# Kernel tuning notes

Measured on AMD Instinct MI355X. Metric: run time of the kernel, lower is better.

## Reference

```python
import jax, jax.numpy as jnp
import numpy as np
from jax.ops import segment_sum, segment_max

N = 40000   # total nodes
E = 160000  # directed edges (before self-loops)
B = 1024    # graphs in batch
FXD = 78    # node feature dim
H = 10      # GAT heads
DOUT = 128  # fc_g1 output dim
DP = 256    # protein feature dim


def setup_inputs() -> dict:
    key = jax.random.key(0)
    ks = jax.random.split(key, 32)
    w = lambda i, shape: jax.random.normal(ks[i], shape, dtype=jnp.float32) * 0.05
    inp = {}
    inp['x'] = jax.random.normal(ks[0], (N, FXD), dtype=jnp.float32)
    inp['edge_index'] = jax.random.randint(ks[1], (2, E), 0, N)
    inp['batch'] = jnp.sort(jax.random.randint(ks[2], (N,), 0, B))
    inp['protein_vec'] = jax.random.normal(ks[3], (B, 1, DP), dtype=jnp.float32)
    # protein_fc
    inp['pfc_w'] = w(4, (DP, DP)); inp['pfc_b'] = w(5, (DP,))
    # GATConv(78 -> 78, heads=10, concat)
    inp['gat_w'] = w(6, (FXD, H * FXD))
    inp['gat_att_src'] = w(7, (H, FXD)); inp['gat_att_dst'] = w(8, (H, FXD))
    inp['gat_b'] = w(9, (H * FXD,))
    # GCNConv(780 -> 780)
    inp['gcn_w'] = w(10, (H * FXD, H * FXD)); inp['gcn_b'] = w(11, (H * FXD,))
    # fc_g1 780 -> 128
    inp['fcg1_w'] = w(12, (H * FXD, DOUT)); inp['fcg1_b'] = w(13, (DOUT,))
    # cross attention projections (d_head = 128)
    inp['q_w'] = w(14, (DOUT, 128)); inp['q_b'] = w(15, (128,))
    inp['k_w'] = w(16, (DP, 128)); inp['k_b'] = w(17, (128,))
    inp['v_w'] = w(18, (DP, DOUT)); inp['v_b'] = w(19, (DOUT,))
    # head MLP
    inp['fc1_w'] = w(20, (DOUT + DP, 1024)); inp['fc1_b'] = w(21, (1024,))
    inp['fc2_w'] = w(22, (1024, 512)); inp['fc2_b'] = w(23, (512,))
    inp['out_w'] = w(24, (512, 1)); inp['out_b'] = w(25, (1,))
    return inp


def _add_self_loops(edge_index):
    loops = jnp.arange(N)
    src = jnp.concatenate([edge_index[0], loops])
    dst = jnp.concatenate([edge_index[1], loops])
    return src, dst


def _gat_conv(x, src, dst, W, a_src, a_dst, b):
    # PyG GATConv: per-head linear, edge attention softmax over dst neighborhoods
    h = (x @ W).reshape(N, H, FXD)                     # [N,H,C]
    asrc = (h * a_src).sum(-1)                          # [N,H]
    adst = (h * a_dst).sum(-1)                          # [N,H]
    alpha = jax.nn.leaky_relu(asrc[src] + adst[dst], 0.2)  # [Etot,H]
    m = segment_max(alpha, dst, num_segments=N)
    e = jnp.exp(alpha - m[dst])
    s = segment_sum(e, dst, num_segments=N)
    attn = e / (s[dst] + 1e-16)
    out = segment_sum(attn[:, :, None] * h[src], dst, num_segments=N)
    return out.reshape(N, H * FXD) + b


def _gcn_conv(x, src, dst, W, b):
    # PyG GCNConv with self-loops and symmetric normalization
    deg = segment_sum(jnp.ones_like(dst, dtype=x.dtype), dst, num_segments=N)
    dinv = jnp.where(deg > 0, deg ** -0.5, 0.0)
    norm = dinv[src] * dinv[dst]                        # [Etot]
    h = x @ W
    return segment_sum(norm[:, None] * h[src], dst, num_segments=N) + b


def reference(x, edge_index, batch, protein_vec, pfc_w, pfc_b, gat_w, gat_att_src,
              gat_att_dst, gat_b, gcn_w, gcn_b, fcg1_w, fcg1_b, q_w, q_b, k_w, k_b,
              v_w, v_b, fc1_w, fc1_b, fc2_w, fc2_b, out_w, out_b):
    relu = jax.nn.relu
    src, dst = _add_self_loops(edge_index)
    pv = relu(protein_vec.squeeze(1) @ pfc_w + pfc_b)   # [B,256] (dropout = eval identity)
    h = relu(_gat_conv(x, src, dst, gat_w, gat_att_src, gat_att_dst, gat_b))
    drug_nodes = relu(_gcn_conv(h, src, dst, gcn_w, gcn_b))          # [N,780]
    dn = relu(drug_nodes @ fcg1_w + fcg1_b)                           # [N,128]
    # cross attention: per-node score against its graph's protein vector
    q = dn @ q_w + q_b                                  # [N,128]
    k = pv @ k_w + k_b                                  # [B,128]
    v = pv @ v_w + v_b                                  # [B,128]
    scores = (q * k[batch]).sum(1, keepdims=True) / jnp.sqrt(128.0)   # [N,1]
    m = segment_max(scores, batch, num_segments=B)
    e = jnp.exp(scores - m[batch])
    s = segment_sum(e, batch, num_segments=B)
    attn = e / s[batch]
    attended = dn + attn * v[batch]                     # [N,128]
    pooled = segment_max(attended, batch, num_segments=B)             # [B,128]
    pooled = jnp.where(jnp.isfinite(pooled), pooled, 0.0)
    xc = jnp.concatenate([pooled, pv], axis=1)          # [B,384]
    h1 = relu(xc @ fc1_w + fc1_b)
    h2 = relu(h1 @ fc2_w + fc2_b)
    return h2 @ out_w + out_b                           # [B,1]
```

## Files before the change

kernel.cpp:

```cpp
#include <hip/hip_runtime.h>
#include <hip/hip_bf16.h>
#include <math.h>

#define N_NODES 40000
#define E_EDGES 160000
#define ETOT    (E_EDGES + N_NODES)
#define B_GRAPH 1024
#define FXD     78
#define H_HEADS 10
#define HF      (H_HEADS * FXD)
#define HF_LD   800
#define XK_LD   96
#define DOUT    128
#define DP      256
#define SCAN_TILES 40

typedef __hip_bfloat16 bf16;
typedef __attribute__((ext_vector_type(8))) short short8;
typedef __attribute__((ext_vector_type(4))) float f32x4;

static __device__ __forceinline__ void storev(float* p, float v) { *p = v; }
static __device__ __forceinline__ void storev(bf16* p, float v) { *p = __float2bfloat16(v); }

static __device__ __forceinline__ ushort f2b_bits(float v) {
    bf16 b = __float2bfloat16(v);
    return *reinterpret_cast<ushort*>(&b);
}
static __device__ __forceinline__ float b2f_bits(short u) {
    return __uint_as_float(((unsigned)(unsigned short)u) << 16);
}

__global__ void k_f2b_pad(const float* __restrict__ in, bf16* __restrict__ out,
                          int M, int K, int ldk) {
    int i = blockIdx.x * blockDim.x + threadIdx.x;
    if (i >= M * ldk) return;
    int r = i / ldk, k = i - r * ldk;
    out[i] = __float2bfloat16((k < K) ? in[(size_t)r * K + k] : 0.f);
}

__global__ void k_f2bt_t(const float* __restrict__ w, bf16* __restrict__ wt,
                         int K, int N, int ldk) {
    __shared__ float tile[32][33];
    const int kt = blockIdx.x * 32;
    const int nt = blockIdx.y * 32;
    const int tx = threadIdx.x & 31, ty = threadIdx.x >> 5;
#pragma unroll
    for (int i = 0; i < 32; i += 8) {
        int k = kt + ty + i, n = nt + tx;
        tile[ty + i][tx] = (k < K && n < N) ? w[(size_t)k * N + n] : 0.f;
    }
    __syncthreads();
#pragma unroll
    for (int i = 0; i < 32; i += 8) {
        int n = nt + ty + i, k = kt + tx;
        if (n < N && k < ldk) wt[(size_t)n * ldk + k] = __float2bfloat16(tile[tx][ty + i]);
    }
}

__global__ void k_eff(const float* __restrict__ gat_w, const float* __restrict__ aw_s,
                      const float* __restrict__ aw_d, bf16* __restrict__ wt_E) {
    int idx = blockIdx.x * blockDim.x + threadIdx.x;
    if (idx >= 20 * XK_LD) return;
    int row = idx / XK_LD, f = idx - row * XK_LD;
    float acc = 0.f;
    if (f < FXD) {
        int h = row % H_HEADS;
        const float* aw = (row < H_HEADS) ? aw_s : aw_d;
        const float* wp = gat_w + (size_t)f * HF + h * FXD;
        const float* ap = aw + h * FXD;
        for (int c = 0; c < FXD; c++) acc += wp[c] * ap[c];
    }
    wt_E[idx] = __float2bfloat16(acc);
}

template <typename OutT, int BIAS, int RELU>
__global__ __launch_bounds__(256)
void mfma_mm(const ushort* __restrict__ A, int lda, const ushort* __restrict__ WT, int ldb,
             const float* __restrict__ bias, OutT* __restrict__ C, int ldc,
             int M, int K, int N) {
    const int RT = (M + 127) >> 7;
    const int CT = (N + 127) >> 7;
    const int p = blockIdx.x;
    const int r = (p & 7) + 8 * (p / (8 * CT));
    const int c = (p >> 3) % CT;
    if (r >= RT) return;
    const int m0 = r * 128;
    const int n0 = c * 128;

    __shared__ ushort As[128 * 40];
    __shared__ ushort Bs[128 * 40];
    const int tid = threadIdx.x;
    const int wave = tid >> 6, lane = tid & 63;
    const int quad = lane >> 4, l16 = lane & 15;
    const int wr = (wave & 1) * 64;
    const int wc = (wave >> 1) * 64;

    f32x4 acc[4][4];
#pragma unroll
    for (int mi = 0; mi < 4; mi++)
#pragma unroll
        for (int ni = 0; ni < 4; ni++) acc[mi][ni] = (f32x4){0.f, 0.f, 0.f, 0.f};

    const int ar = tid >> 1;
    const int ak = (tid & 1) * 16;

    int grow = m0 + ar; if (grow >= M) grow = M - 1;
    int gn   = n0 + ar; if (gn >= N)   gn = N - 1;
    const ushort* arow = A  + (size_t)grow * lda + ak;
    const ushort* brow = WT + (size_t)gn * ldb + ak;

    uint4 a0 = *(const uint4*)(arow);
    uint4 a1 = *(const uint4*)(arow + 8);
    uint4 b0 = *(const uint4*)(brow);
    uint4 b1 = *(const uint4*)(brow + 8);

    for (int kb = 0; kb < K; kb += 32) {
        *(uint4*)&As[ar * 40 + ak]     = a0;
        *(uint4*)&As[ar * 40 + ak + 8] = a1;
        *(uint4*)&Bs[ar * 40 + ak]     = b0;
        *(uint4*)&Bs[ar * 40 + ak + 8] = b1;
        __syncthreads();
        if (kb + 32 < K) {
            a0 = *(const uint4*)(arow + kb + 32);
            a1 = *(const uint4*)(arow + kb + 40);
            b0 = *(const uint4*)(brow + kb + 32);
            b1 = *(const uint4*)(brow + kb + 40);
        }
        short8 af[4], bfr[4];
#pragma unroll
        for (int mi = 0; mi < 4; mi++)
            af[mi] = *(const short8*)&As[(wr + mi * 16 + l16) * 40 + quad * 8];
#pragma unroll
        for (int ni = 0; ni < 4; ni++)
            bfr[ni] = *(const short8*)&Bs[(wc + ni * 16 + l16) * 40 + quad * 8];
#pragma unroll
        for (int mi = 0; mi < 4; mi++)
#pragma unroll
            for (int ni = 0; ni < 4; ni++)
                acc[mi][ni] = __builtin_amdgcn_mfma_f32_16x16x32_bf16(
                    af[mi], bfr[ni], acc[mi][ni], 0, 0, 0);
        __syncthreads();
    }
#pragma unroll
    for (int mi = 0; mi < 4; mi++)
#pragma unroll
        for (int ni = 0; ni < 4; ni++)
#pragma unroll
            for (int rg = 0; rg < 4; rg++) {
                int row = m0 + wr + mi * 16 + quad * 4 + rg;
                int col = n0 + wc + ni * 16 + l16;
                if (row < M && col < N) {
                    float v = acc[mi][ni][rg];
                    if (BIAS) v += bias[col];
                    if (RELU) v = fmaxf(v, 0.f);
                    storev(&C[(size_t)row * ldc + col], v);
                }
            }
}

static inline int mm_grid(int M, int N) {
    int RT = (M + 127) >> 7, CT = (N + 127) >> 7;
    int RTpad = ((RT + 7) >> 3) << 3;
    return RTpad * CT;
}

template <typename OutT, int BIAS, int RELU>
__global__ __launch_bounds__(256)
void mfma_mm64(const ushort* __restrict__ A, int lda, const ushort* __restrict__ WT, int ldb,
               const float* __restrict__ bias, OutT* __restrict__ C, int ldc,
               int M, int K, int N) {
    const int RT = (M + 63) >> 6;
    const int CT = (N + 127) >> 7;
    const int p = blockIdx.x;
    const int r = (p & 7) + 8 * (p / (8 * CT));
    const int c = (p >> 3) % CT;
    if (r >= RT) return;
    const int m0 = r * 64;
    const int n0 = c * 128;

    __shared__ ushort As[64 * 40];
    __shared__ ushort Bs[128 * 40];
    const int tid = threadIdx.x;
    const int wave = tid >> 6, lane = tid & 63;
    const int quad = lane >> 4, l16 = lane & 15;
    const int wc = wave * 32;

    f32x4 acc[4][2];
#pragma unroll
    for (int mi = 0; mi < 4; mi++)
#pragma unroll
        for (int ni = 0; ni < 2; ni++) acc[mi][ni] = (f32x4){0.f, 0.f, 0.f, 0.f};

    const int ar  = tid >> 2, aak = (tid & 3) * 8;
    const int br  = tid >> 1, bak = (tid & 1) * 16;

    int grow = m0 + ar; if (grow >= M) grow = M - 1;
    int gn   = n0 + br; if (gn >= N)   gn = N - 1;
    const ushort* arow = A  + (size_t)grow * lda + aak;
    const ushort* brow = WT + (size_t)gn * ldb + bak;

    uint4 a0 = *(const uint4*)(arow);
    uint4 b0 = *(const uint4*)(brow);
    uint4 b1 = *(const uint4*)(brow + 8);

    for (int kb = 0; kb < K; kb += 32) {
        *(uint4*)&As[ar * 40 + aak]     = a0;
        *(uint4*)&Bs[br * 40 + bak]     = b0;
        *(uint4*)&Bs[br * 40 + bak + 8] = b1;
        __syncthreads();
        if (kb + 32 < K) {
            a0 = *(const uint4*)(arow + kb + 32);
            b0 = *(const uint4*)(brow + kb + 32);
            b1 = *(const uint4*)(brow + kb + 40);
        }
        short8 af[4], bfr[2];
#pragma unroll
        for (int mi = 0; mi < 4; mi++)
            af[mi] = *(const short8*)&As[(mi * 16 + l16) * 40 + quad * 8];
#pragma unroll
        for (int ni = 0; ni < 2; ni++)
            bfr[ni] = *(const short8*)&Bs[(wc + ni * 16 + l16) * 40 + quad * 8];
#pragma unroll
        for (int mi = 0; mi < 4; mi++)
#pragma unroll
            for (int ni = 0; ni < 2; ni++)
                acc[mi][ni] = __builtin_amdgcn_mfma_f32_16x16x32_bf16(
                    af[mi], bfr[ni], acc[mi][ni], 0, 0, 0);
        __syncthreads();
    }
#pragma unroll
    for (int mi = 0; mi < 4; mi++)
#pragma unroll
        for (int ni = 0; ni < 2; ni++)
#pragma unroll
            for (int rg = 0; rg < 4; rg++) {
                int row = m0 + mi * 16 + quad * 4 + rg;
                int col = n0 + wc + ni * 16 + l16;
                if (row < M && col < N) {
                    float v = acc[mi][ni][rg];
                    if (BIAS) v += bias[col];
                    if (RELU) v = fmaxf(v, 0.f);
                    storev(&C[(size_t)row * ldc + col], v);
                }
            }
}

static inline int mm_grid64(int M, int N) {
    int RT = (M + 63) >> 6, CT = (N + 127) >> 7;
    int RTpad = ((RT + 7) >> 3) << 3;
    return RTpad * CT;
}

__global__ void k_pv(const float* __restrict__ pvec, const float* __restrict__ w,
                     const float* __restrict__ b, float* __restrict__ pv) {
    __shared__ float sm[DP];
    int bg = blockIdx.x, t = threadIdx.x;
    sm[t] = pvec[(size_t)bg * DP + t];
    __syncthreads();
    float acc = 0.f;
    for (int k = 0; k < DP; k++) acc += sm[k] * w[(size_t)k * DP + t];
    pv[(size_t)bg * DP + t] = fmaxf(acc + b[t], 0.f);
}

__global__ void k_kv(const float* __restrict__ pv,
                     const float* __restrict__ kw, const float* __restrict__ kb,
                     const float* __restrict__ vw, const float* __restrict__ vb,
                     float* __restrict__ kbuf, float* __restrict__ vbuf) {
    __shared__ float sm[DP];
    int bg = blockIdx.x, t = threadIdx.x;
    sm[t] = pv[(size_t)bg * DP + t];
    __syncthreads();
    int o = t & 127;
    const float* w = (t < 128) ? kw : vw;
    const float* bb = (t < 128) ? kb : vb;
    float acc = 0.f;
    for (int k = 0; k < DP; k++) acc += sm[k] * w[(size_t)k * 128 + o];
    float v = acc + bb[o];
    if (t < 128) kbuf[(size_t)bg * 128 + o] = v;
    else         vbuf[(size_t)bg * 128 + o] = v;
}

__global__ void k_kq(const float* __restrict__ qw, const float* __restrict__ qb,
                     const float* __restrict__ kbuf, float* __restrict__ kq,
                     float* __restrict__ qbk) {
    __shared__ float kb[128];
    int b = blockIdx.x, t = threadIdx.x;
    kb[t] = kbuf[(size_t)b * 128 + t];
    __syncthreads();
    float acc = 0.f;
    for (int o = 0; o < 128; o++) acc += qw[(size_t)t * 128 + o] * kb[o];
    kq[(size_t)b * 128 + t] = acc;
    if (t == 0) {
        float s = 0.f;
        for (int o = 0; o < 128; o++) s += qb[o] * kb[o];
        qbk[b] = s;
    }
}

__global__ void k_count(const int* __restrict__ ei, int* __restrict__ cnt) {
    int e = blockIdx.x * blockDim.x + threadIdx.x;
    if (e >= ETOT) return;
    int d = (e < E_EDGES) ? ei[E_EDGES + e] : e - E_EDGES;
    atomicAdd(&cnt[d], 1);
}

__global__ void k_scan_tile(const int* __restrict__ cnt, int* __restrict__ tile_sums) {
    __shared__ int sm[256];
    int b = blockIdx.x, t = threadIdx.x;
    int idx = b * 1024 + t * 4;
    int4 v = {0, 0, 0, 0};
    if (idx + 3 < N_NODES) v = *(const int4*)(cnt + idx);
    else {
        v.x = (idx     < N_NODES) ? cnt[idx]     : 0;
        v.y = (idx + 1 < N_NODES) ? cnt[idx + 1] : 0;
        v.z = (idx + 2 < N_NODES) ? cnt[idx + 2] : 0;
        v.w = (idx + 3 < N_NODES) ? cnt[idx + 3] : 0;
    }
    sm[t] = v.x + v.y + v.z + v.w;
    __syncthreads();
    for (int off = 128; off > 0; off >>= 1) {
        if (t < off) sm[t] += sm[t + off];
        __syncthreads();
    }
    if (t == 0) tile_sums[b] = sm[0];
}

__global__ void k_scan_top(const int* __restrict__ tile_sums, int* __restrict__ tile_off,
                           int* __restrict__ rowptr) {
    if (threadIdx.x == 0) {
        int run = 0;
        for (int i = 0; i < SCAN_TILES; i++) { tile_off[i] = run; run += tile_sums[i]; }
        rowptr[N_NODES] = run;
    }
}

__global__ void k_scan_write(const int* __restrict__ cnt, const int* __restrict__ tile_off,
                             int* __restrict__ rowptr, int* __restrict__ cursor) {
    __shared__ int sm[256];
    int b = blockIdx.x, t = threadIdx.x;
    int idx = b * 1024 + t * 4;
    int4 v = {0, 0, 0, 0};
    if (idx + 3 < N_NODES) v = *(const int4*)(cnt + idx);
    else {
        v.x = (idx     < N_NODES) ? cnt[idx]     : 0;
        v.y = (idx + 1 < N_NODES) ? cnt[idx + 1] : 0;
        v.z = (idx + 2 < N_NODES) ? cnt[idx + 2] : 0;
        v.w = (idx + 3 < N_NODES) ? cnt[idx + 3] : 0;
    }
    int tsum = v.x + v.y + v.z + v.w;
    sm[t] = tsum;
    __syncthreads();
    for (int off = 1; off < 256; off <<= 1) {
        int add = (t >= off) ? sm[t - off] : 0;
        __syncthreads();
        sm[t] += add;
        __syncthreads();
    }
    int toff = tile_off[b] + sm[t] - tsum;
    int e0 = toff, e1 = e0 + v.x, e2 = e1 + v.y, e3 = e2 + v.z;
    if (idx     < N_NODES) { rowptr[idx]     = e0; cursor[idx]     = e0; }
    if (idx + 1 < N_NODES) { rowptr[idx + 1] = e1; cursor[idx + 1] = e1; }
    if (idx + 2 < N_NODES) { rowptr[idx + 2] = e2; cursor[idx + 2] = e2; }
    if (idx + 3 < N_NODES) { rowptr[idx + 3] = e3; cursor[idx + 3] = e3; }
}

__global__ void k_scatter(const int* __restrict__ ei, int* __restrict__ cursor,
                          int* __restrict__ slist) {
    int e = blockIdx.x * blockDim.x + threadIdx.x;
    if (e >= ETOT) return;
    int s, d;
    if (e < E_EDGES) { s = ei[e]; d = ei[E_EDGES + e]; }
    else             { s = d = e - E_EDGES; }
    int pos = atomicAdd(&cursor[d], 1);
    slist[pos] = s;
}

__global__ void k_dinv(const int* __restrict__ cnt, float* __restrict__ dinv) {
    int n = blockIdx.x * blockDim.x + threadIdx.x;
    if (n >= N_NODES) return;
    int c = cnt[n];
    dinv[n] = (c > 0) ? 1.0f / sqrtf((float)c) : 0.f;
}

__global__ void k_gstart(const int* __restrict__ batch, int* __restrict__ gstart) {
    int n = blockIdx.x * blockDim.x + threadIdx.x;
    if (n >= N_NODES) return;
    int b = batch[n];
    int bp = (n == 0) ? -1 : batch[n - 1];
    for (int g = bp + 1; g <= b; g++) gstart[g] = n;
    if (n == N_NODES - 1)
        for (int g = b + 1; g <= B_GRAPH; g++) gstart[g] = N_NODES;
}

__global__ __launch_bounds__(256)
void k_gat_fused(const int* __restrict__ rowptr, const int* __restrict__ slist,
                 const bf16* __restrict__ h, const float* __restrict__ aa,
                 const float* __restrict__ bias, bf16* __restrict__ outb) {
    const int tid = threadIdx.x;
    const int w = tid >> 6, lane = tid & 63;
    const int d = blockIdx.x * 4 + w;
    const int beg = rowptr[d], end = rowptr[d + 1];

    const float adst_l = (lane < H_HEADS) ? aa[(size_t)d * 20 + 10 + lane] : 0.f;

    const int cA = lane * 8;
    const int cB = (lane + 64) * 8;
    const bool hasB = cB < HF_LD;
    int hloA = cA / FXD;       if (hloA > 9) hloA = 9;
    int hhiA = (cA + 7) / FXD; if (hhiA > 9) hhiA = 9;
    int hloB = cB / FXD;       if (hloB > 9) hloB = 9;
    int hhiB = (cB + 7) / FXD; if (hhiB > 9) hhiB = 9;
    bool selA[8], selB[8];
#pragma unroll
    for (int j = 0; j < 8; j++) {
        int ha = (cA + j) / FXD; if (ha > 9) ha = 9;
        int hb = (cB + j) / FXD; if (hb > 9) hb = 9;
        selA[j] = (ha != hloA);
        selB[j] = (hb != hloB);
    }
    float accA[8], accB[8];
#pragma unroll
    for (int j = 0; j < 8; j++) { accA[j] = 0.f; accB[j] = 0.f; }
    float s_l = 0.f;

    const ushort* hb16 = (const ushort*)h;

    int s_cur = (beg < end) ? slist[beg] : 0;
    short8 va_cur = {0,0,0,0,0,0,0,0}, vb_cur = {0,0,0,0,0,0,0,0};
    float a_cur = 0.f;
    if (beg < end) {
        const ushort* hr = hb16 + (size_t)s_cur * HF_LD;
        va_cur = *(const short8*)(hr + cA);
        if (hasB) vb_cur = *(const short8*)(hr + cB);
        if (lane < H_HEADS) a_cur = aa[(size_t)s_cur * 20 + lane];
    }

    for (int i = beg; i < end; i++) {
        int s_nxt = (i + 1 < end) ? slist[i + 1] : s_cur;
        const ushort* hrn = hb16 + (size_t)s_nxt * HF_LD;
        short8 va_n = *(const short8*)(hrn + cA);
        short8 vb_n = vb_cur;
        if (hasB) vb_n = *(const short8*)(hrn + cB);
        float a_n = 0.f;
        if (lane < H_HEADS) a_n = aa[(size_t)s_nxt * 20 + lane];

        float ex = 0.f;
        if (lane < H_HEADS) {
            float a = a_cur + adst_l;
            a = (a >= 0.f) ? a : 0.2f * a;
            ex = expf(a);
            s_l += ex;
        }
        float exloA = __shfl(ex, hloA), exhiA = __shfl(ex, hhiA);
#pragma unroll
        for (int j = 0; j < 8; j++)
            accA[j] += (selA[j] ? exhiA : exloA) * b2f_bits(va_cur[j]);
        if (hasB) {
            float exloB = __shfl(ex, hloB), exhiB = __shfl(ex, hhiB);
#pragma unroll
            for (int j = 0; j < 8; j++)
                accB[j] += (selB[j] ? exhiB : exloB) * b2f_bits(vb_cur[j]);
        }
        va_cur = va_n; vb_cur = vb_n; a_cur = a_n; s_cur = s_nxt;
    }
    float sinv_l = 1.f / (s_l + 1e-16f);

    ushort* orow = (ushort*)outb + (size_t)d * HF_LD;
    {
        float silo = __shfl(sinv_l, hloA), sihi = __shfl(sinv_l, hhiA);
        union { ushort u[8]; uint4 q; } pk;
#pragma unroll
        for (int j = 0; j < 8; j++) {
            float bz = (cA + j < HF) ? bias[cA + j] : 0.f;
            pk.u[j] = f2b_bits(fmaxf(accA[j] * (selA[j] ? sihi : silo) + bz, 0.f));
        }
        *(uint4*)(orow + cA) = pk.q;
    }
    if (hasB) {
        float silo = __shfl(sinv_l, hloB), sihi = __shfl(sinv_l, hhiB);
        union { ushort u[8]; uint4 q; } pk;
#pragma unroll
        for (int j = 0; j < 8; j++) {
            float bz = (cB + j < HF) ? bias[cB + j] : 0.f;
            pk.u[j] = f2b_bits(fmaxf(accB[j] * (selB[j] ? sihi : silo) + bz, 0.f));
        }
        *(uint4*)(orow + cB) = pk.q;
    }
}

__global__ __launch_bounds__(256)
void k_gcn_aggr_v(const int* __restrict__ rowptr, const int* __restrict__ slist,
                  const bf16* __restrict__ hg,
                  const float* __restrict__ dinv, const float* __restrict__ bias,
                  bf16* __restrict__ outb) {
    const int tid = threadIdx.x;
    const int w = tid >> 6, lane = tid & 63;
    const int d = blockIdx.x * 4 + w;
    const float dv = dinv[d];
    const int cA = lane * 8;
    const int cB = (lane + 64) * 8;
    const bool hasB = cB < HF_LD;
    float accA[8], accB[8];
#pragma unroll
    for (int j = 0; j < 8; j++) { accA[j] = 0.f; accB[j] = 0.f; }
    const int beg = rowptr[d], end = rowptr[d + 1];
    const ushort* hb16 = (const ushort*)hg;

    int s_cur = (beg < end) ? slist[beg] : 0;
    short8 va_cur = {0,0,0,0,0,0,0,0}, vb_cur = {0,0,0,0,0,0,0,0};
    float w_cur = 0.f;
    if (beg < end) {
        const ushort* hr = hb16 + (size_t)s_cur * HF_LD;
        va_cur = *(const short8*)(hr + cA);
        if (hasB) vb_cur = *(const short8*)(hr + cB);
        w_cur = dinv[s_cur] * dv;
    }

    for (int i = beg; i < end; i++) {
        int s_nxt = (i + 1 < end) ? slist[i + 1] : s_cur;
        const ushort* hrn = hb16 + (size_t)s_nxt * HF_LD;
        short8 va_n = *(const short8*)(hrn + cA);
        short8 vb_n = vb_cur;
        if (hasB) vb_n = *(const short8*)(hrn + cB);
        float w_n = dinv[s_nxt] * dv;

#pragma unroll
        for (int j = 0; j < 8; j++) accA[j] += w_cur * b2f_bits(va_cur[j]);
        if (hasB) {
#pragma unroll
            for (int j = 0; j < 8; j++) accB[j] += w_cur * b2f_bits(vb_cur[j]);
        }
        va_cur = va_n; vb_cur = vb_n; w_cur = w_n; s_cur = s_nxt;
    }
    ushort* orow = (ushort*)outb + (size_t)d * HF_LD;
    {
        union { ushort u[8]; uint4 q; } pk;
#pragma unroll
        for (int j = 0; j < 8; j++) {
            float bz = (cA + j < HF) ? bias[cA + j] : 0.f;
            pk.u[j] = f2b_bits(fmaxf(accA[j] + bz, 0.f));
        }
        *(uint4*)(orow + cA) = pk.q;
    }
    if (hasB) {
        union { ushort u[8]; uint4 q; } pk;
#pragma unroll
        for (int j = 0; j < 8; j++) {
            float bz = (cB + j < HF) ? bias[cB + j] : 0.f;
            pk.u[j] = f2b_bits(fmaxf(accB[j] + bz, 0.f));
        }
        *(uint4*)(orow + cB) = pk.q;
    }
}

__global__ void k_scores_e(const float* __restrict__ dn, const float* __restrict__ kq,
                           const float* __restrict__ qbk, const int* __restrict__ batch,
                           float* __restrict__ enode, float* __restrict__ sB) {
    int wv = (blockIdx.x * blockDim.x + threadIdx.x) >> 6;
    int lane = threadIdx.x & 63;
    if (wv >= N_NODES) return;
    int b = batch[wv];
    const float* dp = dn + (size_t)wv * DOUT;
    const float* kp = kq + (size_t)b * DOUT;
    float p = dp[lane] * kp[lane] + dp[lane + 64] * kp[lane + 64];
    for (int off = 32; off > 0; off >>= 1) p += __shfl_down(p, off);
    if (lane == 0) {
        float ex = expf((p + qbk[b]) * 0.08838834764831845f);
        enode[wv] = ex;
        atomicAdd(&sB[b], ex);
    }
}

__global__ __launch_bounds__(384)
void k_pool_xc(const float* __restrict__ dn, const float* __restrict__ vbuf,
               const float* __restrict__ enode, const float* __restrict__ sB,
               const int* __restrict__ gstart, const float* __restrict__ pv,
               bf16* __restrict__ xcb) {
    int g = blockIdx.x, t = threadIdx.x;
    if (t < 128) {
        int s0 = gstart[g], s1 = gstart[g + 1];
        float inv = 1.f / sB[g];
        float vb = vbuf[(size_t)g * 128 + t];
        float m = -3.4e38f;
        for (int n = s0; n < s1; n++)
            m = fmaxf(m, dn[(size_t)n * 128 + t] + (enode[n] * inv) * vb);
        xcb[(size_t)g * 384 + t] = __float2bfloat16((s1 > s0) ? m : 0.f);
    } else {
        xcb[(size_t)g * 384 + t] = __float2bfloat16(pv[(size_t)g * DP + (t - 128)]);
    }
}

__global__ void k_out(const float* __restrict__ h2, const float* __restrict__ ow,
                      const float* __restrict__ ob, float* __restrict__ out) {
    int row = (blockIdx.x * blockDim.x + threadIdx.x) >> 6;
    int lane = threadIdx.x & 63;
    if (row >= B_GRAPH) return;
    float p = 0.f;
    for (int j = lane; j < 512; j += 64) p += h2[(size_t)row * 512 + j] * ow[j];
    for (int off = 32; off > 0; off >>= 1) p += __shfl_down(p, off);
    if (lane == 0) out[row] = p + ob[0];
}

__global__ void k_fail(float* __restrict__ out, int n) {
    int i = blockIdx.x * blockDim.x + threadIdx.x;
    if (i < n) out[i] = 12345.0f;
}

extern "C" void kernel_launch(void* const* d_in, const int* in_sizes, int n_in,
                              void* d_out, int out_size, void* d_ws, size_t ws_size,
                              hipStream_t stream) {
    const float* x        = (const float*)d_in[0];
    const int*   ei       = (const int*)d_in[1];
    const int*   batch    = (const int*)d_in[2];
    const float* pvec     = (const float*)d_in[3];
    const float* pfc_w    = (const float*)d_in[4];
    const float* pfc_b    = (const float*)d_in[5];
    const float* gat_w    = (const float*)d_in[6];
    const float* gat_asrc = (const float*)d_in[7];
    const float* gat_adst = (const float*)d_in[8];
    const float* gat_b    = (const float*)d_in[9];
    const float* gcn_w    = (const float*)d_in[10];
    const float* gcn_b    = (const float*)d_in[11];
    const float* fcg1_w   = (const float*)d_in[12];
    const float* fcg1_b   = (const float*)d_in[13];
    const float* q_w      = (const float*)d_in[14];
    const float* q_b      = (const float*)d_in[15];
    const float* k_w      = (const float*)d_in[16];
    const float* k_b      = (const float*)d_in[17];
    const float* v_w      = (const float*)d_in[18];
    const float* v_b      = (const float*)d_in[19];
    const float* fc1_w    = (const float*)d_in[20];
    const float* fc1_b    = (const float*)d_in[21];
    const float* fc2_w    = (const float*)d_in[22];
    const float* fc2_b    = (const float*)d_in[23];
    const float* out_w    = (const float*)d_in[24];
    const float* out_b    = (const float*)d_in[25];
    float* out = (float*)d_out;

    char* base = (char*)d_ws;
    size_t off = 0;
    auto alloc = [&](size_t bytes) -> void* {
        void* r = base + off;
        off += (bytes + 255) & ~(size_t)255;
        return r;
    };
    float*    pv      = (float*)alloc((size_t)B_GRAPH * DP * 4);
    bf16*     xb      = (bf16*)alloc((size_t)N_NODES * XK_LD * 2);
    bf16*     wt_gat  = (bf16*)alloc((size_t)HF * XK_LD * 2);
    bf16*     wt_gcn  = (bf16*)alloc((size_t)HF * HF_LD * 2);
    bf16*     wt_fcg1 = (bf16*)alloc((size_t)DOUT * HF_LD * 2);
    bf16*     wt_fc1  = (bf16*)alloc((size_t)1024 * 384 * 2);
    bf16*     wt_fc2  = (bf16*)alloc((size_t)512 * 1024 * 2);
    bf16*     wt_E    = (bf16*)alloc((size_t)20 * XK_LD * 2);
    bf16*     hB      = (bf16*)alloc((size_t)N_NODES * HF_LD * 2);
    bf16*     g1      = (bf16*)alloc((size_t)N_NODES * HF_LD * 2);
    float*    aa      = (float*)alloc((size_t)N_NODES * 20 * 4);
    int*      cnt     = (int*)alloc((size_t)N_NODES * 4);
    int*      rowptr  = (int*)alloc((size_t)(N_NODES + 1) * 4);
    int*      cursor  = (int*)alloc((size_t)N_NODES * 4);
    int*      slist   = (int*)alloc((size_t)ETOT * 4);
    int*      tsums   = (int*)alloc((size_t)SCAN_TILES * 4);
    int*      toff    = (int*)alloc((size_t)SCAN_TILES * 4);
    int*      gstart  = (int*)alloc((size_t)(B_GRAPH + 1) * 4);
    float*    dinv    = (float*)alloc((size_t)N_NODES * 4);
    float*    dn      = (float*)alloc((size_t)N_NODES * DOUT * 4);
    float*    kbuf    = (float*)alloc((size_t)B_GRAPH * 128 * 4);
    float*    vbuf    = (float*)alloc((size_t)B_GRAPH * 128 * 4);
    float*    kq      = (float*)alloc((size_t)B_GRAPH * 128 * 4);
    float*    qbk     = (float*)alloc((size_t)B_GRAPH * 4);
    float*    enode   = (float*)alloc((size_t)N_NODES * 4);
    float*    sB      = (float*)alloc((size_t)B_GRAPH * 4);
    bf16*     xcb     = (bf16*)alloc((size_t)B_GRAPH * 384 * 2);
    bf16*     h1b     = (bf16*)alloc((size_t)B_GRAPH * 1024 * 2);
    float*    h2      = (float*)alloc((size_t)B_GRAPH * 512 * 4);

    if (off > ws_size) {
        k_fail<<<(out_size + 255) / 256, 256, 0, stream>>>(out, out_size);
        return;
    }

    (void)hipMemsetAsync(cnt, 0, (size_t)N_NODES * 4, stream);
    (void)hipMemsetAsync(sB, 0, (size_t)B_GRAPH * 4, stream);

    k_f2b_pad<<<(N_NODES * XK_LD + 255) / 256, 256, 0, stream>>>(x, xb, N_NODES, FXD, XK_LD);
    k_eff<<<(20 * XK_LD + 255) / 256, 256, 0, stream>>>(gat_w, gat_asrc, gat_adst, wt_E);
    {
        dim3 g1t((XK_LD + 31) / 32, (HF + 31) / 32);
        k_f2bt_t<<<g1t, 256, 0, stream>>>(gat_w, wt_gat, FXD, HF, XK_LD);
        dim3 g2t((HF_LD + 31) / 32, (HF + 31) / 32);
        k_f2bt_t<<<g2t, 256, 0, stream>>>(gcn_w, wt_gcn, HF, HF, HF_LD);
        dim3 g3t((HF_LD + 31) / 32, (DOUT + 31) / 32);
        k_f2bt_t<<<g3t, 256, 0, stream>>>(fcg1_w, wt_fcg1, HF, DOUT, HF_LD);
        dim3 g4t((384 + 31) / 32, (1024 + 31) / 32);
        k_f2bt_t<<<g4t, 256, 0, stream>>>(fc1_w, wt_fc1, 384, 1024, 384);
        dim3 g5t((1024 + 31) / 32, (512 + 31) / 32);
        k_f2bt_t<<<g5t, 256, 0, stream>>>(fc2_w, wt_fc2, 1024, 512, 1024);
    }

    k_pv<<<B_GRAPH, 256, 0, stream>>>(pvec, pfc_w, pfc_b, pv);
    k_kv<<<B_GRAPH, 256, 0, stream>>>(pv, k_w, k_b, v_w, v_b, kbuf, vbuf);
    k_kq<<<B_GRAPH, 128, 0, stream>>>(q_w, q_b, kbuf, kq, qbk);

    k_count<<<(ETOT + 255) / 256, 256, 0, stream>>>(ei, cnt);
    k_scan_tile<<<SCAN_TILES, 256, 0, stream>>>(cnt, tsums);
    k_scan_top<<<1, 64, 0, stream>>>(tsums, toff, rowptr);
    k_scan_write<<<SCAN_TILES, 256, 0, stream>>>(cnt, toff, rowptr, cursor);
    k_scatter<<<(ETOT + 255) / 256, 256, 0, stream>>>(ei, cursor, slist);
    k_dinv<<<(N_NODES + 255) / 256, 256, 0, stream>>>(cnt, dinv);
    k_gstart<<<(N_NODES + 255) / 256, 256, 0, stream>>>(batch, gstart);

    mfma_mm64<float, 0, 0><<<mm_grid64(N_NODES, 20), 256, 0, stream>>>(
        (const ushort*)xb, XK_LD, (const ushort*)wt_E, XK_LD, nullptr, aa, 20,
        N_NODES, XK_LD, 20);
    mfma_mm<bf16, 0, 0><<<mm_grid(N_NODES, HF), 256, 0, stream>>>(
        (const ushort*)xb, XK_LD, (const ushort*)wt_gat, XK_LD, nullptr, hB, HF_LD,
        N_NODES, XK_LD, HF);
    k_gat_fused<<<N_NODES / 4, 256, 0, stream>>>(rowptr, slist, hB, aa, gat_b, g1);

    mfma_mm<bf16, 0, 0><<<mm_grid(N_NODES, HF), 256, 0, stream>>>(
        (const ushort*)g1, HF_LD, (const ushort*)wt_gcn, HF_LD, nullptr, hB, HF_LD,
        N_NODES, HF_LD, HF);
    k_gcn_aggr_v<<<N_NODES / 4, 256, 0, stream>>>(rowptr, slist, hB, dinv, gcn_b, g1);

    mfma_mm64<float, 1, 1><<<mm_grid64(N_NODES, DOUT), 256, 0, stream>>>(
        (const ushort*)g1, HF_LD, (const ushort*)wt_fcg1, HF_LD, fcg1_b, dn, DOUT,
        N_NODES, HF_LD, DOUT);

    k_scores_e<<<(N_NODES * 64 + 255) / 256, 256, 0, stream>>>(dn, kq, qbk, batch,
                                                               enode, sB);
    k_pool_xc<<<B_GRAPH, 384, 0, stream>>>(dn, vbuf, enode, sB, gstart, pv, xcb);

    mfma_mm64<bf16, 1, 1><<<mm_grid64(B_GRAPH, 1024), 256, 0, stream>>>(
        (const ushort*)xcb, 384, (const ushort*)wt_fc1, 384, fc1_b, h1b, 1024,
        B_GRAPH, 384, 1024);
    mfma_mm64<float, 1, 1><<<mm_grid64(B_GRAPH, 512), 256, 0, stream>>>(
        (const ushort*)h1b, 1024, (const ushort*)wt_fc2, 1024, fc2_b, h2, 512,
        B_GRAPH, 1024, 512);
    k_out<<<(B_GRAPH * 64 + 255) / 256, 256, 0, stream>>>(h2, out_w, out_b, out);
}
```

Before: 551.4 us.

## Merge prep kernels into one launch, fold dinv/gstart into scan, store dn as bf16

Folds the input cast, the five weight transposes, the attention-weight precompute and the two memsets into a single k_prep launch using block-range dispatch. dinv and gstart are now computed inside k_scan_write, which removes two more launches. The fc_g1 output dn is stored in bf16 and read as packed pairs in the scores and pooling kernels, halving that intermediate's traffic. The intent is to cut launch overhead and memory bandwidth, at the cost of lower precision for dn and a pooling kernel that leaves half its threads idle.

```diff
diff --git a/kernel.cpp b/kernel.cpp
--- a/kernel.cpp
+++ b/kernel.cpp
@@ -30,19 +30,10 @@
     return __uint_as_float(((unsigned)(unsigned short)u) << 16);
 }
 
-__global__ void k_f2b_pad(const float* __restrict__ in, bf16* __restrict__ out,
-                          int M, int K, int ldk) {
-    int i = blockIdx.x * blockDim.x + threadIdx.x;
-    if (i >= M * ldk) return;
-    int r = i / ldk, k = i - r * ldk;
-    out[i] = __float2bfloat16((k < K) ? in[(size_t)r * K + k] : 0.f);
-}
-
-__global__ void k_f2bt_t(const float* __restrict__ w, bf16* __restrict__ wt,
-                         int K, int N, int ldk) {
-    __shared__ float tile[32][33];
-    const int kt = blockIdx.x * 32;
-    const int nt = blockIdx.y * 32;
+static __device__ void t_tile(const float* __restrict__ w, bf16* __restrict__ wt,
+                              int K, int N, int ldk, int ktile, int ntile,
+                              float (*tile)[33]) {
+    const int kt = ktile * 32, nt = ntile * 32;
     const int tx = threadIdx.x & 31, ty = threadIdx.x >> 5;
 #pragma unroll
     for (int i = 0; i < 32; i += 8) {
@@ -57,20 +48,70 @@
     }
 }
 
-__global__ void k_eff(const float* __restrict__ gat_w, const float* __restrict__ aw_s,
-                      const float* __restrict__ aw_d, bf16* __restrict__ wt_E) {
-    int idx = blockIdx.x * blockDim.x + threadIdx.x;
-    if (idx >= 20 * XK_LD) return;
-    int row = idx / XK_LD, f = idx - row * XK_LD;
-    float acc = 0.f;
-    if (f < FXD) {
-        int h = row % H_HEADS;
-        const float* aw = (row < H_HEADS) ? aw_s : aw_d;
-        const float* wp = gat_w + (size_t)f * HF + h * FXD;
-        const float* ap = aw + h * FXD;
-        for (int c = 0; c < FXD; c++) acc += wp[c] * ap[c];
-    }
-    wt_E[idx] = __float2bfloat16(acc);
+__global__ __launch_bounds__(256)
+void k_prep(const float* __restrict__ x, const float* __restrict__ gat_w,
+            const float* __restrict__ gcn_w, const float* __restrict__ fcg1_w,
+            const float* __restrict__ fc1_w, const float* __restrict__ fc2_w,
+            const float* __restrict__ aw_s, const float* __restrict__ aw_d,
+            bf16* __restrict__ xb, bf16* __restrict__ wt_gat, bf16* __restrict__ wt_gcn,
+            bf16* __restrict__ wt_fcg1, bf16* __restrict__ wt_fc1, bf16* __restrict__ wt_fc2,
+            bf16* __restrict__ wt_E, int* __restrict__ cnt, float* __restrict__ sB) {
+    __shared__ float tile[32][33];
+    int p = blockIdx.x;
+    const int NB_XB  = (N_NODES * XK_LD + 255) / 256;
+    const int TGAT   = 3 * 25;
+    const int TGCN   = 25 * 25;
+    const int TFCG   = 25 * 4;
+    const int TFC1   = 12 * 32;
+    const int TFC2   = 32 * 16;
+    const int NB_E   = (20 * XK_LD + 255) / 256;
+    const int NB_CNT = (N_NODES + 255) / 256;
+
+    if (p < NB_XB) {
+        int i = p * 256 + threadIdx.x;
+        if (i < N_NODES * XK_LD) {
+            int r = i / XK_LD, k = i - r * XK_LD;
+            xb[i] = __float2bfloat16((k < FXD) ? x[(size_t)r * FXD + k] : 0.f);
+        }
+        return;
+    }
+    p -= NB_XB;
+    if (p < TGAT)  { t_tile(gat_w,  wt_gat,  FXD,  HF,   XK_LD, p % 3,  p / 3,  tile); return; }
+    p -= TGAT;
+    if (p < TGCN)  { t_tile(gcn_w,  wt_gcn,  HF,   HF,   HF_LD, p % 25, p / 25, tile); return; }
+    p -= TGCN;
+    if (p < TFCG)  { t_tile(fcg1_w, wt_fcg1, HF,   DOUT, HF_LD, p % 25, p / 25, tile); return; }
+    p -= TFCG;
+    if (p < TFC1)  { t_tile(fc1_w,  wt_fc1,  384,  1024, 384,   p % 12, p / 12, tile); return; }
+    p -= TFC1;
+    if (p < TFC2)  { t_tile(fc2_w,  wt_fc2,  1024, 512,  1024,  p % 32, p / 32, tile); return; }
+    p -= TFC2;
+    if (p < NB_E) {
+        int idx = p * 256 + threadIdx.x;
+        if (idx < 20 * XK_LD) {
+            int row = idx / XK_LD, f = idx - row * XK_LD;
+            float acc = 0.f;
+            if (f < FXD) {
+                int h = row % H_HEADS;
+                const float* aw = (row < H_HEADS) ? aw_s : aw_d;
+                const float* wp = gat_w + (size_t)f * HF + h * FXD;
+                const float* ap = aw + h * FXD;
+                for (int c = 0; c < FXD; c++) acc += wp[c] * ap[c];
+            }
+            wt_E[idx] = __float2bfloat16(acc);
+        }
+        return;
+    }
+    p -= NB_E;
+    if (p < NB_CNT) {
+        int i = p * 256 + threadIdx.x;
+        if (i < N_NODES) cnt[i] = 0;
+        if (p == 0 && threadIdx.x == 0) { }
+        return;
+    }
+    p -= NB_CNT;
+    int i = p * 256 + threadIdx.x;
+    if (i < B_GRAPH) sB[i] = 0.f;
 }
 
 template <typename OutT, int BIAS, int RELU>
@@ -335,7 +376,9 @@
 }
 
 __global__ void k_scan_write(const int* __restrict__ cnt, const int* __restrict__ tile_off,
-                             int* __restrict__ rowptr, int* __restrict__ cursor) {
+                             const int* __restrict__ batch,
+                             int* __restrict__ rowptr, int* __restrict__ cursor,
+                             float* __restrict__ dinv, int* __restrict__ gstart) {
     __shared__ int sm[256];
     int b = blockIdx.x, t = threadIdx.x;
     int idx = b * 1024 + t * 4;
@@ -362,6 +405,18 @@
     if (idx + 1 < N_NODES) { rowptr[idx + 1] = e1; cursor[idx + 1] = e1; }
     if (idx + 2 < N_NODES) { rowptr[idx + 2] = e2; cursor[idx + 2] = e2; }
     if (idx + 3 < N_NODES) { rowptr[idx + 3] = e3; cursor[idx + 3] = e3; }
+    int cc[4] = {v.x, v.y, v.z, v.w};
+#pragma unroll
+    for (int j = 0; j < 4; j++) {
+        int n = idx + j;
+        if (n >= N_NODES) break;
+        dinv[n] = (cc[j] > 0) ? 1.0f / sqrtf((float)cc[j]) : 0.f;
+        int bg = batch[n];
+        int bp = (n == 0) ? -1 : batch[n - 1];
+        for (int g = bp + 1; g <= bg; g++) gstart[g] = n;
+        if (n == N_NODES - 1)
+            for (int g = bg + 1; g <= B_GRAPH; g++) gstart[g] = N_NODES;
+    }
 }
 
 __global__ void k_scatter(const int* __restrict__ ei, int* __restrict__ cursor,
@@ -373,23 +428,6 @@
     else             { s = d = e - E_EDGES; }
     int pos = atomicAdd(&cursor[d], 1);
     slist[pos] = s;
-}
-
-__global__ void k_dinv(const int* __restrict__ cnt, float* __restrict__ dinv) {
-    int n = blockIdx.x * blockDim.x + threadIdx.x;
-    if (n >= N_NODES) return;
-    int c = cnt[n];
-    dinv[n] = (c > 0) ? 1.0f / sqrtf((float)c) : 0.f;
-}
-
-__global__ void k_gstart(const int* __restrict__ batch, int* __restrict__ gstart) {
-    int n = blockIdx.x * blockDim.x + threadIdx.x;
-    if (n >= N_NODES) return;
-    int b = batch[n];
-    int bp = (n == 0) ? -1 : batch[n - 1];
-    for (int g = bp + 1; g <= b; g++) gstart[g] = n;
-    if (n == N_NODES - 1)
-        for (int g = b + 1; g <= B_GRAPH; g++) gstart[g] = N_NODES;
 }
 
 __global__ __launch_bounds__(256)
@@ -553,16 +591,18 @@
     }
 }
 
-__global__ void k_scores_e(const float* __restrict__ dn, const float* __restrict__ kq,
+__global__ void k_scores_e(const bf16* __restrict__ dnb, const float* __restrict__ kq,
                            const float* __restrict__ qbk, const int* __restrict__ batch,
                            float* __restrict__ enode, float* __restrict__ sB) {
     int wv = (blockIdx.x * blockDim.x + threadIdx.x) >> 6;
     int lane = threadIdx.x & 63;
     if (wv >= N_NODES) return;
     int b = batch[wv];
-    const float* dp = dn + (size_t)wv * DOUT;
+    const ushort* dp = (const ushort*)dnb + (size_t)wv * DOUT;
     const float* kp = kq + (size_t)b * DOUT;
-    float p = dp[lane] * kp[lane] + dp[lane + 64] * kp[lane + 64];
+    uint dd = *(const uint*)(dp + lane * 2);
+    float p = b2f_bits((ushort)dd) * kp[lane * 2]
+            + b2f_bits((ushort)(dd >> 16)) * kp[lane * 2 + 1];
     for (int off = 32; off > 0; off >>= 1) p += __shfl_down(p, off);
     if (lane == 0) {
         float ex = expf((p + qbk[b]) * 0.08838834764831845f);
@@ -572,20 +612,28 @@
 }
 
 __global__ __launch_bounds__(384)
-void k_pool_xc(const float* __restrict__ dn, const float* __restrict__ vbuf,
+void k_pool_xc(const bf16* __restrict__ dnb, const float* __restrict__ vbuf,
                const float* __restrict__ enode, const float* __restrict__ sB,
                const int* __restrict__ gstart, const float* __restrict__ pv,
                bf16* __restrict__ xcb) {
     int g = blockIdx.x, t = threadIdx.x;
-    if (t < 128) {
+    if (t < 64) {
         int s0 = gstart[g], s1 = gstart[g + 1];
         float inv = 1.f / sB[g];
-        float vb = vbuf[(size_t)g * 128 + t];
-        float m = -3.4e38f;
-        for (int n = s0; n < s1; n++)
-            m = fmaxf(m, dn[(size_t)n * 128 + t] + (enode[n] * inv) * vb);
-        xcb[(size_t)g * 384 + t] = __float2bfloat16((s1 > s0) ? m : 0.f);
-    } else {
+        float vb0 = vbuf[(size_t)g * 128 + 2 * t];
+        float vb1 = vbuf[(size_t)g * 128 + 2 * t + 1];
+        float m0 = -3.4e38f, m1 = -3.4e38f;
+        const ushort* dp = (const ushort*)dnb;
+        for (int n = s0; n < s1; n++) {
+            uint dd = *(const uint*)(dp + (size_t)n * 128 + 2 * t);
+            float a = enode[n] * inv;
+            m0 = fmaxf(m0, b2f_bits((ushort)dd) + a * vb0);
+            m1 = fmaxf(m1, b2f_bits((ushort)(dd >> 16)) + a * vb1);
+        }
+        bool ne = s1 > s0;
+        xcb[(size_t)g * 384 + 2 * t]     = __float2bfloat16(ne ? m0 : 0.f);
+        xcb[(size_t)g * 384 + 2 * t + 1] = __float2bfloat16(ne ? m1 : 0.f);
+    } else if (t >= 128) {
         xcb[(size_t)g * 384 + t] = __float2bfloat16(pv[(size_t)g * DP + (t - 128)]);
     }
 }
@@ -663,7 +711,7 @@
     int*      toff    = (int*)alloc((size_t)SCAN_TILES * 4);
     int*      gstart  = (int*)alloc((size_t)(B_GRAPH + 1) * 4);
     float*    dinv    = (float*)alloc((size_t)N_NODES * 4);
-    float*    dn      = (float*)alloc((size_t)N_NODES * DOUT * 4);
+    bf16*     dnb     = (bf16*)alloc((size_t)N_NODES * DOUT * 2);
     float*    kbuf    = (float*)alloc((size_t)B_GRAPH * 128 * 4);
     float*    vbuf    = (float*)alloc((size_t)B_GRAPH * 128 * 4);
     float*    kq      = (float*)alloc((size_t)B_GRAPH * 128 * 4);
@@ -679,22 +727,16 @@
         return;
     }
 
-    (void)hipMemsetAsync(cnt, 0, (size_t)N_NODES * 4, stream);
-    (void)hipMemsetAsync(sB, 0, (size_t)B_GRAPH * 4, stream);
-
-    k_f2b_pad<<<(N_NODES * XK_LD + 255) / 256, 256, 0, stream>>>(x, xb, N_NODES, FXD, XK_LD);
-    k_eff<<<(20 * XK_LD + 255) / 256, 256, 0, stream>>>(gat_w, gat_asrc, gat_adst, wt_E);
     {
-        dim3 g1t((XK_LD + 31) / 32, (HF + 31) / 32);
-        k_f2bt_t<<<g1t, 256, 0, stream>>>(gat_w, wt_gat, FXD, HF, XK_LD);
-        dim3 g2t((HF_LD + 31) / 32, (HF + 31) / 32);
-        k_f2bt_t<<<g2t, 256, 0, stream>>>(gcn_w, wt_gcn, HF, HF, HF_LD);
-        dim3 g3t((HF_LD + 31) / 32, (DOUT + 31) / 32);
-        k_f2bt_t<<<g3t, 256, 0, stream>>>(fcg1_w, wt_fcg1, HF, DOUT, HF_LD);
-        dim3 g4t((384 + 31) / 32, (1024 + 31) / 32);
-        k_f2bt_t<<<g4t, 256, 0, stream>>>(fc1_w, wt_fc1, 384, 1024, 384);
-        dim3 g5t((1024 + 31) / 32, (512 + 31) / 32);
-        k_f2bt_t<<<g5t, 256, 0, stream>>>(fc2_w, wt_fc2, 1024, 512, 1024);
+        int nb = (N_NODES * XK_LD + 255) / 256
+               + 3 * 25 + 25 * 25 + 25 * 4 + 12 * 32 + 32 * 16
+               + (20 * XK_LD + 255) / 256
+               + (N_NODES + 255) / 256
+               + (B_GRAPH + 255) / 256;
+        k_prep<<<nb, 256, 0, stream>>>(x, gat_w, gcn_w, fcg1_w, fc1_w, fc2_w,
+                                       gat_asrc, gat_adst,
+                                       xb, wt_gat, wt_gcn, wt_fcg1, wt_fc1, wt_fc2,
+                                       wt_E, cnt, sB);
     }
 
     k_pv<<<B_GRAPH, 256, 0, stream>>>(pvec, pfc_w, pfc_b, pv);
@@ -704,10 +746,9 @@
     k_count<<<(ETOT + 255) / 256, 256, 0, stream>>>(ei, cnt);
     k_scan_tile<<<SCAN_TILES, 256, 0, stream>>>(cnt, tsums);
     k_scan_top<<<1, 64, 0, stream>>>(tsums, toff, rowptr);
-    k_scan_write<<<SCAN_TILES, 256, 0, stream>>>(cnt, toff, rowptr, cursor);
+    k_scan_write<<<SCAN_TILES, 256, 0, stream>>>(cnt, toff, batch, rowptr, cursor,
+                                                 dinv, gstart);
     k_scatter<<<(ETOT + 255) / 256, 256, 0, stream>>>(ei, cursor, slist);
-    k_dinv<<<(N_NODES + 255) / 256, 256, 0, stream>>>(cnt, dinv);
-    k_gstart<<<(N_NODES + 255) / 256, 256, 0, stream>>>(batch, gstart);
 
     mfma_mm64<float, 0, 0><<<mm_grid64(N_NODES, 20), 256, 0, stream>>>(
         (const ushort*)xb, XK_LD, (const ushort*)wt_E, XK_LD, nullptr, aa, 20,
@@ -722,13 +763,13 @@
         N_NODES, HF_LD, HF);
     k_gcn_aggr_v<<<N_NODES / 4, 256, 0, stream>>>(rowptr, slist, hB, dinv, gcn_b, g1);
 
-    mfma_mm64<float, 1, 1><<<mm_grid64(N_NODES, DOUT), 256, 0, stream>>>(
-        (const ushort*)g1, HF_LD, (const ushort*)wt_fcg1, HF_LD, fcg1_b, dn, DOUT,
+    mfma_mm64<bf16, 1, 1><<<mm_grid64(N_NODES, DOUT), 256, 0, stream>>>(
+        (const ushort*)g1, HF_LD, (const ushort*)wt_fcg1, HF_LD, fcg1_b, dnb, DOUT,
         N_NODES, HF_LD, DOUT);
 
-    k_scores_e<<<(N_NODES * 64 + 255) / 256, 256, 0, stream>>>(dn, kq, qbk, batch,
+    k_scores_e<<<(N_NODES * 64 + 255) / 256, 256, 0, stream>>>(dnb, kq, qbk, batch,
                                                                enode, sB);
-    k_pool_xc<<<B_GRAPH, 384, 0, stream>>>(dn, vbuf, enode, sB, gstart, pv, xcb);
+    k_pool_xc<<<B_GRAPH, 384, 0, stream>>>(dnb, vbuf, enode, sB, gstart, pv, xcb);
 
     mfma_mm64<bf16, 1, 1><<<mm_grid64(B_GRAPH, 1024), 256, 0, stream>>>(
         (const ushort*)xcb, 384, (const ushort*)wt_fc1, 384, fc1_b, h1b, 1024,
```

Measured after the change: 533.4 us. -3.3%, faster.
